# Kernel tuning notes

Measured on AMD Instinct MI355X. Metric: run time of the kernel, lower is better.

## Reference

```python
import jax, jax.numpy as jnp
import numpy as np

ALPHA = 0.01  # leaky relu negative slope


def _leaky(x):
    return jnp.where(x >= 0, x, ALPHA * x)


def setup_inputs() -> dict:
    key = jax.random.key(0)
    ks = jax.random.split(key, 8)
    B, N, Fin, Fout = 2, 1024, 64, 32
    inp = jax.random.normal(ks[0], (B, N, Fin), dtype=jnp.float32)
    k = jax.random.normal(ks[1], (B, N, Fin), dtype=jnp.float32)
    v = jax.random.normal(ks[2], (B, N, Fin), dtype=jnp.float32)
    adj = jax.random.uniform(ks[3], (N, N), dtype=jnp.float32)
    W = jax.random.normal(ks[4], (Fin, Fout), dtype=jnp.float32) * 0.1
    Wk = jax.random.normal(ks[5], (Fin, Fout), dtype=jnp.float32) * 0.1
    Wv = jax.random.normal(ks[6], (Fin, Fout), dtype=jnp.float32) * 0.1
    a = jax.random.normal(ks[7], (2 * Fout, 1), dtype=jnp.float32) * 0.1
    return {"inp": inp, "k": k, "v": v, "adj": adj, "W": W, "Wk": Wk, "Wv": Wv, "a": a}


def reference(inp, k, v, adj, W, Wk, Wv, a):
    # Projections
    h = jnp.matmul(inp, W)   # [B, N, F]
    kk = jnp.matmul(k, Wk)   # [B, N, F]
    vv = jnp.matmul(v, Wv)   # [B, N, F]
    B, N, F = h.shape
    # Faithful replication of the original (buggy) concat along dim=1 + view.
    th = jnp.tile(h, (1, 1, N)).reshape(B, N * N, F)   # row m=i*N+j -> h[:, i]
    tk = jnp.tile(kk, (1, N, 1))                       # row m -> k[:, m % N]
    cat = jnp.concatenate([th, tk], axis=1)            # [B, 2*N*N, F]
    cat = cat.reshape(B, N, N, 2 * F)                  # row-major reinterp (matches torch .view)
    scores = _leaky(jnp.einsum('bijc,co->bij', cat, a))  # [B, N, N]
    att = jax.nn.softmax(scores, axis=-1)
    # dropout is identity (eval mode, p=0.0)
    out = jnp.matmul((att + adj[None, :, :]) * 0.5, vv)  # [B, N, F]
    return _leaky(out)  # concat=True path
```

## Files before the change

### kernel.cpp

```cpp
#include <hip/hip_runtime.h>


#define ALPHA 0.01f

__device__ __forceinline__ float leaky(float x){ return x >= 0.f ? x : ALPHA*x; }

__global__ __launch_bounds__(256) void k_proj(
    const float* __restrict__ inp, const float* __restrict__ kin,
    const float* __restrict__ vin, const float* __restrict__ W,
    const float* __restrict__ Wk,  const float* __restrict__ Wv,
    const float* __restrict__ a,
    float* __restrict__ vv, float* __restrict__ p,
    float* __restrict__ q1, float* __restrict__ q2)
{
    int tid  = threadIdx.x;
    int lane = tid & 63;
    int f    = lane & 31;
    int h    = lane >> 5;
    int rl   = tid >> 6;
    int row  = blockIdx.x*4 + rl;
    const float* xr = inp + row*64 + h*32;
    const float* kr = kin + row*64 + h*32;
    const float* vr = vin + row*64 + h*32;
    const float* Wb  = W  + (h*32)*32 + f;
    const float* Wkb = Wk + (h*32)*32 + f;
    const float* Wvb = Wv + (h*32)*32 + f;
    float ha = 0.f, ka = 0.f, va = 0.f;
    #pragma unroll
    for (int c = 0; c < 32; c++){
        float x = xr[c], k = kr[c], v = vr[c];
        ha += x * Wb [c*32];
        ka += k * Wkb[c*32];
        va += v * Wvb[c*32];
    }
    ha += __shfl_xor(ha, 32);
    ka += __shfl_xor(ka, 32);
    va += __shfl_xor(va, 32);
    if (h == 0) vv[row*32 + f] = va;
    float a1 = a[f], a2 = a[32+f];
    float pv  = ha*(a1+a2);
    float q1v = ka*a1;
    float q2v = ka*a2;
    #pragma unroll
    for (int m = 16; m; m >>= 1){
        pv  += __shfl_xor(pv , m);
        q1v += __shfl_xor(q1v, m);
        q2v += __shfl_xor(q2v, m);
    }
    if (lane == 0){ p[row] = pv; q1[row] = q1v; q2[row] = q2v; }
}

__global__ __launch_bounds__(256) void k_fused(
    const float* __restrict__ adj, const float* __restrict__ vv,
    const float* __restrict__ p,   const float* __restrict__ q1,
    const float* __restrict__ q2,  float* __restrict__ out)
{
    __shared__ float e[1024];
    __shared__ float accred[4][4][32];
    __shared__ float raccred[4][32];
    __shared__ float vsred[4][32];
    __shared__ float zred[4];

    int tid = threadIdx.x;
    int b   = blockIdx.x & 1;
    int it  = blockIdx.x >> 1;
    int o   = tid & 7;
    int rr  = (tid >> 3) & 3;
    int js  = tid >> 5;
    int w   = tid >> 6;
    int i   = it*4 + rr;

    const float* q1b = q1 + b*1024;
    const float* q2b = q2 + b*1024;
    float zsum = 0.f;
    #pragma unroll
    for (int t = 0; t < 4; t++){
        int j  = tid*4 + t;
        float s = leaky(q1b[(2*j) & 1023] + q2b[(2*j+1) & 1023]);
        float ev = __expf(s);
        e[j] = ev;
        zsum += ev;
    }
    #pragma unroll
    for (int m = 32; m; m >>= 1) zsum += __shfl_xor(zsum, m);
    if ((tid & 63) == 0) zred[w] = zsum;
    __syncthreads();

    const float4* ap = (const float4*)(adj + i*1024 + js*128);
    const float4* ep = (const float4*)(e + js*128);
    const float*  vb = vv + b*32768 + js*128*32 + o*4;
    float4 acc  = make_float4(0.f,0.f,0.f,0.f);
    float4 racc = make_float4(0.f,0.f,0.f,0.f);
    float4 vs   = make_float4(0.f,0.f,0.f,0.f);
    #pragma unroll 4
    for (int m = 0; m < 32; m++){
        float4 a4 = ap[m];
        float4 e4 = ep[m];
        const float* v0p = vb + m*128;
        float4 v0 = *(const float4*)(v0p);
        float4 v1 = *(const float4*)(v0p + 32);
        float4 v2 = *(const float4*)(v0p + 64);
        float4 v3 = *(const float4*)(v0p + 96);
        acc.x += a4.x*v0.x; acc.y += a4.x*v0.y; acc.z += a4.x*v0.z; acc.w += a4.x*v0.w;
        acc.x += a4.y*v1.x; acc.y += a4.y*v1.y; acc.z += a4.y*v1.z; acc.w += a4.y*v1.w;
        acc.x += a4.z*v2.x; acc.y += a4.z*v2.y; acc.z += a4.z*v2.z; acc.w += a4.z*v2.w;
        acc.x += a4.w*v3.x; acc.y += a4.w*v3.y; acc.z += a4.w*v3.z; acc.w += a4.w*v3.w;
        racc.x += e4.x*v0.x; racc.y += e4.x*v0.y; racc.z += e4.x*v0.z; racc.w += e4.x*v0.w;
        racc.x += e4.y*v1.x; racc.y += e4.y*v1.y; racc.z += e4.y*v1.z; racc.w += e4.y*v1.w;
        racc.x += e4.z*v2.x; racc.y += e4.z*v2.y; racc.z += e4.z*v2.z; racc.w += e4.z*v2.w;
        racc.x += e4.w*v3.x; racc.y += e4.w*v3.y; racc.z += e4.w*v3.z; racc.w += e4.w*v3.w;
        vs.x += v0.x + v1.x + v2.x + v3.x;
        vs.y += v0.y + v1.y + v2.y + v3.y;
        vs.z += v0.z + v1.z + v2.z + v3.z;
        vs.w += v0.w + v1.w + v2.w + v3.w;
    }
    acc.x  += __shfl_xor(acc.x, 32);  acc.y  += __shfl_xor(acc.y, 32);
    acc.z  += __shfl_xor(acc.z, 32);  acc.w  += __shfl_xor(acc.w, 32);
    racc.x += __shfl_xor(racc.x, 32); racc.y += __shfl_xor(racc.y, 32);
    racc.z += __shfl_xor(racc.z, 32); racc.w += __shfl_xor(racc.w, 32);
    vs.x   += __shfl_xor(vs.x, 32);   vs.y   += __shfl_xor(vs.y, 32);
    vs.z   += __shfl_xor(vs.z, 32);   vs.w   += __shfl_xor(vs.w, 32);
    if ((tid & 32) == 0){
        accred[w][rr][o*4+0] = acc.x;
        accred[w][rr][o*4+1] = acc.y;
        accred[w][rr][o*4+2] = acc.z;
        accred[w][rr][o*4+3] = acc.w;
        if (rr == 0){
            raccred[w][o*4+0] = racc.x; raccred[w][o*4+1] = racc.y;
            raccred[w][o*4+2] = racc.z; raccred[w][o*4+3] = racc.w;
            vsred[w][o*4+0] = vs.x; vsred[w][o*4+1] = vs.y;
            vsred[w][o*4+2] = vs.z; vsred[w][o*4+3] = vs.w;
        }
    }
    __syncthreads();

    if (tid < 128){
        int rr2 = tid >> 5, f = tid & 31;
        float accsum = accred[0][rr2][f] + accred[1][rr2][f]
                     + accred[2][rr2][f] + accred[3][rr2][f];
        int i2 = it*4 + rr2;
        float att;
        if (i2 < 512){
            float vlo = vsred[0][f] + vsred[1][f];
            float vhi = vsred[2][f] + vsred[3][f];
            float s0 = leaky(p[b*1024 + 2*i2]);
            float s1 = leaky(p[b*1024 + 2*i2 + 1]);
            float e0 = __expf(s0), e1 = __expf(s1);
            att = (e0*vlo + e1*vhi) / (512.f*(e0 + e1));
        } else {
            float rsum = raccred[0][f] + raccred[1][f]
                       + raccred[2][f] + raccred[3][f];
            float Z = zred[0] + zred[1] + zred[2] + zred[3];
            att = rsum / Z;
        }
        out[(b*1024 + i2)*32 + f] = leaky(0.5f*(att + accsum));
    }
}

extern "C" void kernel_launch(void* const* d_in, const int* in_sizes, int n_in,
                              void* d_out, int out_size, void* d_ws, size_t ws_size,
                              hipStream_t stream)
{
    const float* inp = (const float*)d_in[0];
    const float* kin = (const float*)d_in[1];
    const float* vin = (const float*)d_in[2];
    const float* adj = (const float*)d_in[3];
    const float* W   = (const float*)d_in[4];
    const float* Wk  = (const float*)d_in[5];
    const float* Wv  = (const float*)d_in[6];
    const float* a   = (const float*)d_in[7];
    float* out = (float*)d_out;

    float* ws  = (float*)d_ws;
    float* vv  = ws;
    float* p   = ws + 65536;
    float* q1  = ws + 67584;
    float* q2  = ws + 69632;
    (void)in_sizes; (void)n_in; (void)out_size; (void)ws_size;

    hipLaunchKernelGGL(k_proj, dim3(512), dim3(256), 0, stream,
                       inp, kin, vin, W, Wk, Wv, a, vv, p, q1, q2);
    hipLaunchKernelGGL(k_fused, dim3(512), dim3(256), 0, stream,
                       adj, vv, p, q1, q2, out);
}
```

Measured before the change: 94.95 us.

## Merge projection and attention kernels into one cooperative launch with grid sync

Fuses the projection kernel and the fused attention kernel into a single cooperative kernel that uses a grid-wide barrier between the two phases. The aim is to remove the second kernel launch and the gap between the two kernels. In exchange it pays for a grid.sync across 512 blocks and needs every block to be co-resident, which the launch-bounds hint of two blocks per CU is meant to help with. A cooperative launch can also carry its own overhead.

New measurement: 149.5 us. 57.5% more time.

```diff
diff --git a/kernel.cpp b/kernel.cpp
--- a/kernel.cpp
+++ b/kernel.cpp
@@ -1,60 +1,23 @@
 #include <hip/hip_runtime.h>
+#include <hip/hip_cooperative_groups.h>
 
 
 #define ALPHA 0.01f
+namespace cg = cooperative_groups;
 
 __device__ __forceinline__ float leaky(float x){ return x >= 0.f ? x : ALPHA*x; }
 
-__global__ __launch_bounds__(256) void k_proj(
+__global__ __launch_bounds__(256, 2) void gat_one(
     const float* __restrict__ inp, const float* __restrict__ kin,
-    const float* __restrict__ vin, const float* __restrict__ W,
-    const float* __restrict__ Wk,  const float* __restrict__ Wv,
-    const float* __restrict__ a,
+    const float* __restrict__ vin, const float* __restrict__ adj,
+    const float* __restrict__ W,   const float* __restrict__ Wk,
+    const float* __restrict__ Wv,  const float* __restrict__ a,
     float* __restrict__ vv, float* __restrict__ p,
-    float* __restrict__ q1, float* __restrict__ q2)
+    float* __restrict__ q1, float* __restrict__ q2,
+    float* __restrict__ out)
 {
-    int tid  = threadIdx.x;
-    int lane = tid & 63;
-    int f    = lane & 31;
-    int h    = lane >> 5;
-    int rl   = tid >> 6;
-    int row  = blockIdx.x*4 + rl;
-    const float* xr = inp + row*64 + h*32;
-    const float* kr = kin + row*64 + h*32;
-    const float* vr = vin + row*64 + h*32;
-    const float* Wb  = W  + (h*32)*32 + f;
-    const float* Wkb = Wk + (h*32)*32 + f;
-    const float* Wvb = Wv + (h*32)*32 + f;
-    float ha = 0.f, ka = 0.f, va = 0.f;
-    #pragma unroll
-    for (int c = 0; c < 32; c++){
-        float x = xr[c], k = kr[c], v = vr[c];
-        ha += x * Wb [c*32];
-        ka += k * Wkb[c*32];
-        va += v * Wvb[c*32];
-    }
-    ha += __shfl_xor(ha, 32);
-    ka += __shfl_xor(ka, 32);
-    va += __shfl_xor(va, 32);
-    if (h == 0) vv[row*32 + f] = va;
-    float a1 = a[f], a2 = a[32+f];
-    float pv  = ha*(a1+a2);
-    float q1v = ka*a1;
-    float q2v = ka*a2;
-    #pragma unroll
-    for (int m = 16; m; m >>= 1){
-        pv  += __shfl_xor(pv , m);
-        q1v += __shfl_xor(q1v, m);
-        q2v += __shfl_xor(q2v, m);
-    }
-    if (lane == 0){ p[row] = pv; q1[row] = q1v; q2[row] = q2v; }
-}
+    cg::grid_group grid = cg::this_grid();
 
-__global__ __launch_bounds__(256) void k_fused(
-    const float* __restrict__ adj, const float* __restrict__ vv,
-    const float* __restrict__ p,   const float* __restrict__ q1,
-    const float* __restrict__ q2,  float* __restrict__ out)
-{
     __shared__ float e[1024];
     __shared__ float accred[4][4][32];
     __shared__ float raccred[4][32];
@@ -62,6 +25,46 @@
     __shared__ float zred[4];
 
     int tid = threadIdx.x;
+
+    {
+        int lane = tid & 63;
+        int f    = lane & 31;
+        int h    = lane >> 5;
+        int rl   = tid >> 6;
+        int row  = blockIdx.x*4 + rl;
+        const float* xr = inp + row*64 + h*32;
+        const float* kr = kin + row*64 + h*32;
+        const float* vr = vin + row*64 + h*32;
+        const float* Wb  = W  + (h*32)*32 + f;
+        const float* Wkb = Wk + (h*32)*32 + f;
+        const float* Wvb = Wv + (h*32)*32 + f;
+        float ha = 0.f, ka = 0.f, va = 0.f;
+        #pragma unroll
+        for (int c = 0; c < 32; c++){
+            float x = xr[c], k = kr[c], v = vr[c];
+            ha += x * Wb [c*32];
+            ka += k * Wkb[c*32];
+            va += v * Wvb[c*32];
+        }
+        ha += __shfl_xor(ha, 32);
+        ka += __shfl_xor(ka, 32);
+        va += __shfl_xor(va, 32);
+        if (h == 0) vv[row*32 + f] = va;
+        float a1 = a[f], a2 = a[32+f];
+        float pv  = ha*(a1+a2);
+        float q1v = ka*a1;
+        float q2v = ka*a2;
+        #pragma unroll
+        for (int m = 16; m; m >>= 1){
+            pv  += __shfl_xor(pv , m);
+            q1v += __shfl_xor(q1v, m);
+            q2v += __shfl_xor(q2v, m);
+        }
+        if (lane == 0){ p[row] = pv; q1[row] = q1v; q2[row] = q2v; }
+    }
+
+    grid.sync();
+
     int b   = blockIdx.x & 1;
     int it  = blockIdx.x >> 1;
     int o   = tid & 7;
@@ -178,8 +181,12 @@
     float* q2  = ws + 69632;
     (void)in_sizes; (void)n_in; (void)out_size; (void)ws_size;
 
-    hipLaunchKernelGGL(k_proj, dim3(512), dim3(256), 0, stream,
-                       inp, kin, vin, W, Wk, Wv, a, vv, p, q1, q2);
-    hipLaunchKernelGGL(k_fused, dim3(512), dim3(256), 0, stream,
-                       adj, vv, p, q1, q2, out);
+    void* kargs[] = {
+        (void*)&inp, (void*)&kin, (void*)&vin, (void*)&adj,
+        (void*)&W, (void*)&Wk, (void*)&Wv, (void*)&a,
+        (void*)&vv, (void*)&p, (void*)&q1, (void*)&q2,
+        (void*)&out
+    };
+    hipLaunchCooperativeKernel((void*)gat_one, dim3(512), dim3(256),
+                               kargs, 0, stream);
 }
```
